# Optimization experiments

Hardware: AMD Instinct MI355X
Metric: run time of the kernel (lower is better)

## Reference

```python
import jax, jax.numpy as jnp
import numpy as np

B, T, D = 4, 2048, 1024
H = 16
HD = D // H  # 64


def setup_inputs() -> dict:
    key = jax.random.key(0)
    ks = jax.random.split(key, 6)
    s = 0.02
    x = jax.random.normal(ks[0], (B, T, D), dtype=jnp.float32)
    # per-head projection weights, stored stacked: [H, HD, D] (torch Linear weight layout)
    Wq = jax.random.normal(ks[1], (H, HD, D), dtype=jnp.float32) * s
    Wk = jax.random.normal(ks[2], (H, HD, D), dtype=jnp.float32) * s
    Wv = jax.random.normal(ks[3], (H, HD, D), dtype=jnp.float32) * s
    Wo = jax.random.normal(ks[4], (D, D), dtype=jnp.float32) * s  # proj weight [out, in]
    bo = jax.random.normal(ks[5], (D,), dtype=jnp.float32) * s
    return {"x": x, "Wq": Wq, "Wk": Wk, "Wv": Wv, "Wo": Wo, "bo": bo}


def reference(x, Wq, Wk, Wv, Wo, bo):
    Bx, Tx, _ = x.shape
    # project: [B,T,D] x [H,HD,D] -> [B,H,T,HD]
    q = jnp.einsum('btd,hed->bhte', x, Wq)
    k = jnp.einsum('btd,hed->bhte', x, Wk)
    v = jnp.einsum('btd,hed->bhte', x, Wv)
    scale = 1.0 / jnp.sqrt(jnp.array(q.shape[-1], dtype=x.dtype))
    scores = jnp.einsum('bhte,bhse->bhts', q, k) * scale  # [B,H,T,T]
    causal = jnp.tril(jnp.ones((Tx, Tx), dtype=bool))
    scores = jnp.where(causal, scores, jnp.array(-jnp.inf, dtype=scores.dtype))
    weights = jax.nn.softmax(scores, axis=-1)
    out = jnp.einsum('bhts,bhse->bhte', weights, v)  # [B,H,T,HD]
    # concat heads (head h occupies contiguous slice, matching torch.cat order)
    out = out.transpose(0, 2, 1, 3).reshape(Bx, Tx, -1)  # [B,T,D]
    out = out @ Wo.T + bo
    return out
```

## Files before the change

### kernel.cpp

```cpp
#include <hip/hip_runtime.h>
#include <cstdint>
#include <cstddef>

typedef unsigned short u16;
typedef float  f32x4  __attribute__((ext_vector_type(4)));
typedef __bf16 bf16x8 __attribute__((ext_vector_type(8)));
typedef unsigned short us8 __attribute__((ext_vector_type(8)));
typedef unsigned short us4 __attribute__((ext_vector_type(4)));
typedef float  f32x4v __attribute__((ext_vector_type(4)));
typedef unsigned int u32x2 __attribute__((ext_vector_type(2)));

#define AS1 __attribute__((address_space(1)))
#define AS3 __attribute__((address_space(3)))

__device__ __forceinline__ u16 f2b(float f) {
  unsigned u = __float_as_uint(f);
  u += 0x7FFFu + ((u >> 16) & 1u);
  return (u16)(u >> 16);
}

__device__ __forceinline__ unsigned pkbf(float a, float b) {
  unsigned ua = __float_as_uint(a) + 0x8000u;
  unsigned ub = __float_as_uint(b) + 0x8000u;
  return __builtin_amdgcn_perm(ub, ua, 0x07060302u);
}

__device__ __forceinline__ bf16x8 ldfrag(const u16* p) {
  us8 v = *(const us8*)p;
  return __builtin_bit_cast(bf16x8, v);
}

__device__ __forceinline__ f32x4 mfma16(bf16x8 a, bf16x8 b, f32x4 c) {
  return __builtin_amdgcn_mfma_f32_16x16x32_bf16(a, b, c, 0, 0, 0);
}

__device__ __forceinline__ void gl_lds16(const u16* g, AS3 u16* l) {
  __builtin_amdgcn_global_load_lds((AS1 void*)g, (AS3 void*)l, 16, 0, 0);
}


__global__ __launch_bounds__(256) void cvt_all(
    const float* __restrict__ x,
    const float* __restrict__ Wq, const float* __restrict__ Wk,
    const float* __restrict__ Wv, const float* __restrict__ Wo,
    u16* __restrict__ xb, u16* __restrict__ Wqkv, u16* __restrict__ Wob) {
  int blk = blockIdx.x;
  const float* s;
  u16* d;
  int i;
  if (blk < 8192)       { s = x;  d = xb;             i = blk * 256 + threadIdx.x; }
  else if (blk < 9216)  { s = Wq; d = Wqkv;           i = (blk - 8192) * 256 + threadIdx.x; }
  else if (blk < 10240) { s = Wk; d = Wqkv + 1048576; i = (blk - 9216) * 256 + threadIdx.x; }
  else if (blk < 11264) { s = Wv; d = Wqkv + 2097152; i = (blk - 10240) * 256 + threadIdx.x; }
  else                  { s = Wo; d = Wob;            i = (blk - 11264) * 256 + threadIdx.x; }
  f32x4v f = ((const f32x4v*)s)[i];
  us4 o = { f2b(f[0]), f2b(f[1]), f2b(f[2]), f2b(f[3]) };
  ((us4*)d)[i] = o;
}

__global__ __launch_bounds__(256) void gemm_qkv(
    const u16* __restrict__ A, const u16* __restrict__ W,
    u16* __restrict__ Qb, u16* __restrict__ Kb, u16* __restrict__ Vt) {
  __shared__ u16 lA[128 * 32];
  __shared__ u16 lB[128 * 32];
  const int tid = threadIdx.x;
  const int lane = tid & 63, wave = tid >> 6;
  const int quad = lane >> 4, l16 = lane & 15;
  const int wr = wave >> 1, wc = wave & 1;
  const int m0 = blockIdx.y * 128;
  const int n0 = blockIdx.x * 128;
  const int sec = n0 >> 10;
  AS3 u16* lA3 = (AS3 u16*)lA;
  AS3 u16* lB3 = (AS3 u16*)lB;
  f32x4 acc[4][4] = {};
  const int swg = (((tid & 3) ^ ((tid >> 3) & 3)) * 8);
  const int qsw = (quad ^ ((l16 >> 1) & 3)) * 8;
  const int ar0 = m0 + (tid >> 2);
  const int br0 = n0 + (tid >> 2);

  const u16* gA0 = A + (size_t)ar0 * 1024 + swg;
  const u16* gA1 = gA0 + 64 * 1024;
  const u16* gB0 = W + (size_t)br0 * 1024 + swg;
  const u16* gB1 = gB0 + 64 * 1024;

  for (int k0 = 0; k0 < 1024; k0 += 32) {
    __syncthreads();
    gl_lds16(gA0 + k0, lA3 + wave * 512);
    gl_lds16(gA1 + k0, lA3 + 2048 + wave * 512);
    gl_lds16(gB0 + k0, lB3 + wave * 512);
    gl_lds16(gB1 + k0, lB3 + 2048 + wave * 512);
    __syncthreads();
    bf16x8 aF[4], bF[4];
#pragma unroll
    for (int mt = 0; mt < 4; mt++)
      aF[mt] = ldfrag(&lA[(wr * 64 + mt * 16 + l16) * 32 + qsw]);
#pragma unroll
    for (int nt = 0; nt < 4; nt++)
      bF[nt] = ldfrag(&lB[(wc * 64 + nt * 16 + l16) * 32 + qsw]);
    if (sec != 2) {
#pragma unroll
      for (int mt = 0; mt < 4; mt++)
#pragma unroll
        for (int nt = 0; nt < 4; nt++)
          acc[mt][nt] = mfma16(aF[mt], bF[nt], acc[mt][nt]);
    } else {
#pragma unroll
      for (int mt = 0; mt < 4; mt++)
#pragma unroll
        for (int nt = 0; nt < 4; nt++)
          acc[mt][nt] = mfma16(bF[nt], aF[mt], acc[mt][nt]);
    }
  }

  if (sec != 2) {
    const float qs = 0.180336880111120426f;
#pragma unroll
    for (int mt = 0; mt < 4; mt++) {
#pragma unroll
      for (int nt = 0; nt < 4; nt++) {
#pragma unroll
        for (int r = 0; r < 4; r++) {
          float v = acc[mt][nt][r];
          int m = m0 + wr * 64 + mt * 16 + quad * 4 + r;
          int n = n0 + wc * 64 + nt * 16 + l16;
          int ns = n & 1023;
          int h = ns >> 6, e = ns & 63;
          int b = m >> 11, t = m & 2047;
          size_t bh = (size_t)b * 16 + h;
          if (sec == 0) Qb[(bh * 2048 + t) * 64 + e] = f2b(v * qs);
          else          Kb[(bh * 2048 + t) * 64 + e] = f2b(v);
        }
      }
    }
  } else {
#pragma unroll
    for (int mt = 0; mt < 4; mt++) {
#pragma unroll
      for (int nt = 0; nt < 4; nt++) {
#pragma unroll
        for (int r = 0; r < 4; r++) {
          float v = acc[mt][nt][r];
          int n = n0 + wc * 64 + nt * 16 + quad * 4 + r;
          int m = m0 + wr * 64 + mt * 16 + l16;
          int ns = n & 1023;
          int h = ns >> 6, e = ns & 63;
          int b = m >> 11, t = m & 2047;
          size_t bh = (size_t)b * 16 + h;
          Vt[(bh * 64 + e) * 2048 + t] = f2b(v);
        }
      }
    }
  }
}

__global__ __launch_bounds__(512, 4) void attn(
    const u16* __restrict__ Q, const u16* __restrict__ K,
    const u16* __restrict__ Vt, u16* __restrict__ O) {
  __shared__ u16 lK[128 * 72];
  __shared__ u16 lV[64 * 136];
  __shared__ u16 lP[8 * 16 * 40];
  const int tid = threadIdx.x;
  const int lane = tid & 63, wave = tid >> 6;
  const int quad = lane >> 4, l16 = lane & 15;
  const int bh = blockIdx.x;
  const int pidx = blockIdx.y;
  const size_t base = (size_t)bh * (2048 * 64);
  u16* lPw = lP + wave * 640;
  const int b = bh >> 4, h = bh & 15;

  for (int half = 0; half < 2; half++) {
    const int qb = half ? pidx : (15 - pidx);
    const int t0 = qb << 7;
    const int tq = t0 + wave * 16 + l16;
    const bf16x8 qF0 = ldfrag(Q + base + (size_t)tq * 64 + quad * 8);
    const bf16x8 qF1 = ldfrag(Q + base + (size_t)tq * 64 + 32 + quad * 8);
    float m_i = -INFINITY, l_i = 0.f;
    f32x4 o[4] = {};

    for (int j = 0; j <= qb; j++) {
      const int s0 = j << 7;
      __syncthreads();
#pragma unroll
      for (int i = 0; i < 2; i++) {
        int c = tid + i * 512;
        int r = c >> 3, col = (c & 7) * 8;
        *(us8*)&lK[r * 72 + col] = *(const us8*)(K + base + (size_t)(s0 + r) * 64 + col);
      }
#pragma unroll
      for (int i = 0; i < 2; i++) {
        int c = tid + i * 512;
        int e = c >> 4, col = (c & 15) * 8;
        *(us8*)&lV[e * 136 + col] = *(const us8*)(Vt + base + (size_t)e * 2048 + s0 + col);
      }
      __syncthreads();

      f32x4 S[8];
      __builtin_amdgcn_s_setprio(1);
#pragma unroll
      for (int nt = 0; nt < 8; nt++) {
        int sr = nt * 16 + l16;
        f32x4 a = {};
        a = mfma16(ldfrag(&lK[sr * 72 + quad * 8]), qF0, a);
        a = mfma16(ldfrag(&lK[sr * 72 + 32 + quad * 8]), qF1, a);
        S[nt] = a;
      }
      __builtin_amdgcn_s_setprio(0);

      if (j == qb) {
#pragma unroll
        for (int nt = 0; nt < 8; nt++)
#pragma unroll
          for (int r = 0; r < 4; r++) {
            int s = s0 + nt * 16 + quad * 4 + r;
            if (s > tq) S[nt][r] = -INFINITY;
          }
      }

      f32x4 m4 = S[0];
#pragma unroll
      for (int nt = 1; nt < 8; nt++)
#pragma unroll
        for (int r = 0; r < 4; r++) m4[r] = fmaxf(m4[r], S[nt][r]);
      float mx = fmaxf(fmaxf(m4[0], m4[1]), fmaxf(m4[2], m4[3]));
      mx = fmaxf(mx, __shfl_xor(mx, 16));
      mx = fmaxf(mx, __shfl_xor(mx, 32));
      float mn = fmaxf(m_i, mx);
      float alpha = __builtin_amdgcn_exp2f(m_i - mn);
      float sum = 0.f;
#pragma unroll
      for (int nt = 0; nt < 8; nt++)
#pragma unroll
        for (int r = 0; r < 4; r++) {
          float p = __builtin_amdgcn_exp2f(S[nt][r] - mn);
          S[nt][r] = p;
          sum += p;
        }
      sum += __shfl_xor(sum, 16);
      sum += __shfl_xor(sum, 32);
      l_i = l_i * alpha + sum;
      m_i = mn;
#pragma unroll
      for (int ot = 0; ot < 4; ot++)
#pragma unroll
        for (int r = 0; r < 4; r++) o[ot][r] *= alpha;

#pragma unroll
      for (int c = 0; c < 4; c++) {
        u32x2 d0 = { pkbf(S[2*c][0],   S[2*c][1]),   pkbf(S[2*c][2],   S[2*c][3]) };
        u32x2 d1 = { pkbf(S[2*c+1][0], S[2*c+1][1]), pkbf(S[2*c+1][2], S[2*c+1][3]) };
        *(u32x2*)&lPw[l16 * 40 + quad * 4]      = d0;
        *(u32x2*)&lPw[l16 * 40 + 16 + quad * 4] = d1;
        __asm__ volatile("s_waitcnt lgkmcnt(0)" ::: "memory");
        bf16x8 bP = ldfrag(&lPw[l16 * 40 + quad * 8]);
        __builtin_amdgcn_s_setprio(1);
#pragma unroll
        for (int ot = 0; ot < 4; ot++)
          o[ot] = mfma16(ldfrag(&lV[(ot * 16 + l16) * 136 + c * 32 + quad * 8]), bP, o[ot]);
        __builtin_amdgcn_s_setprio(0);
      }
    }

    const float inv = 1.f / l_i;
#pragma unroll
    for (int ot = 0; ot < 4; ot++) {
      u32x2 pk = { pkbf(o[ot][0] * inv, o[ot][1] * inv),
                   pkbf(o[ot][2] * inv, o[ot][3] * inv) };
      *(u32x2*)&O[((size_t)b * 2048 + tq) * 1024 + h * 64 + ot * 16 + quad * 4] = pk;
    }
  }
}

__global__ __launch_bounds__(256) void gemm_out(
    const u16* __restrict__ A, const u16* __restrict__ W,
    const float* __restrict__ bias, float* __restrict__ out) {
  __shared__ u16 lA[128 * 32];
  __shared__ u16 lB[128 * 32];
  const int tid = threadIdx.x;
  const int lane = tid & 63, wave = tid >> 6;
  const int quad = lane >> 4, l16 = lane & 15;
  const int wr = wave >> 1, wc = wave & 1;
  const int m0 = blockIdx.y * 128;
  const int n0 = blockIdx.x * 128;
  AS3 u16* lA3 = (AS3 u16*)lA;
  AS3 u16* lB3 = (AS3 u16*)lB;
  f32x4 acc[4][4] = {};
  const int swg = (((tid & 3) ^ ((tid >> 3) & 3)) * 8);
  const int qsw = (quad ^ ((l16 >> 1) & 3)) * 8;
  const int ar0 = m0 + (tid >> 2);
  const int br0 = n0 + (tid >> 2);
  const u16* gA0 = A + (size_t)ar0 * 1024 + swg;
  const u16* gA1 = gA0 + 64 * 1024;
  const u16* gB0 = W + (size_t)br0 * 1024 + swg;
  const u16* gB1 = gB0 + 64 * 1024;

  for (int k0 = 0; k0 < 1024; k0 += 32) {
    __syncthreads();
    gl_lds16(gA0 + k0, lA3 + wave * 512);
    gl_lds16(gA1 + k0, lA3 + 2048 + wave * 512);
    gl_lds16(gB0 + k0, lB3 + wave * 512);
    gl_lds16(gB1 + k0, lB3 + 2048 + wave * 512);
    __syncthreads();
    bf16x8 aF[4], bF[4];
#pragma unroll
    for (int mt = 0; mt < 4; mt++)
      aF[mt] = ldfrag(&lA[(wr * 64 + mt * 16 + l16) * 32 + qsw]);
#pragma unroll
    for (int nt = 0; nt < 4; nt++)
      bF[nt] = ldfrag(&lB[(wc * 64 + nt * 16 + l16) * 32 + qsw]);
#pragma unroll
    for (int mt = 0; mt < 4; mt++)
#pragma unroll
      for (int nt = 0; nt < 4; nt++)
        acc[mt][nt] = mfma16(aF[mt], bF[nt], acc[mt][nt]);
  }

#pragma unroll
  for (int mt = 0; mt < 4; mt++) {
#pragma unroll
    for (int nt = 0; nt < 4; nt++) {
#pragma unroll
      for (int r = 0; r < 4; r++) {
        int m = m0 + wr * 64 + mt * 16 + quad * 4 + r;
        int n = n0 + wc * 64 + nt * 16 + l16;
        out[(size_t)m * 1024 + n] = acc[mt][nt][r] + bias[n];
      }
    }
  }
}

extern "C" void kernel_launch(void* const* d_in, const int* in_sizes, int n_in,
                              void* d_out, int out_size, void* d_ws, size_t ws_size,
                              hipStream_t stream) {
  const float* x  = (const float*)d_in[0];
  const float* Wq = (const float*)d_in[1];
  const float* Wk = (const float*)d_in[2];
  const float* Wv = (const float*)d_in[3];
  const float* Wo = (const float*)d_in[4];
  const float* bo = (const float*)d_in[5];
  float* out = (float*)d_out;

  u16* ws   = (u16*)d_ws;
  u16* xb   = ws;
  u16* Wqkv = ws + 8388608;
  u16* Wob  = ws + 11534336;
  u16* Qb   = ws + 12582912;
  u16* Ao   = xb;
  u16* Kb   = (u16*)d_out;
  u16* Vt   = Kb + 8388608;

  cvt_all<<<12288, 256, 0, stream>>>(x, Wq, Wk, Wv, Wo, xb, Wqkv, Wob);
  gemm_qkv<<<dim3(24, 64), 256, 0, stream>>>(xb, Wqkv, Qb, Kb, Vt);
  attn<<<dim3(64, 8), 512, 0, stream>>>(Qb, Kb, Vt, Ao);
  gemm_out<<<dim3(8, 64), 256, 0, stream>>>(Ao, Wob, bo, out);
}
```

Measured before the change: 259.1 us.

## Rewrite QKV GEMM as 256x256 double-buffered pipelined kernel with block swizzle

Replaces the 128x128 single-buffered QKV projection GEMM with a 512-thread, 256x256-tile kernel. It uses a 128KB double-buffered LDS staging with k-step 64 and interleaves global->LDS loads with quarter-tile MFMA phases, using explicit waitcnt, barriers and setprio. A 1D grid with an XCD-aware block swizzle replaces the 2D launch. The aim is to raise reuse per tile and hide global load latency behind MFMA work. The cost is more register and LDS pressure, only 384 blocks, and fragile manual scheduling.

```diff
diff --git a/kernel.cpp b/kernel.cpp
--- a/kernel.cpp
+++ b/kernel.cpp
@@ -38,6 +38,10 @@
   __builtin_amdgcn_global_load_lds((AS1 void*)g, (AS3 void*)l, 16, 0, 0);
 }
 
+#define BAR()  do { __builtin_amdgcn_s_barrier(); __builtin_amdgcn_sched_barrier(0); } while (0)
+#define WLG()  do { __asm__ volatile("s_waitcnt lgkmcnt(0)" ::: "memory"); __builtin_amdgcn_sched_barrier(0); } while (0)
+#define WVM4() do { __asm__ volatile("s_waitcnt vmcnt(4)" ::: "memory"); __builtin_amdgcn_sched_barrier(0); } while (0)
+#define WVM0() do { __asm__ volatile("s_waitcnt vmcnt(0)" ::: "memory"); __builtin_amdgcn_sched_barrier(0); } while (0)
 
 __global__ __launch_bounds__(256) void cvt_all(
     const float* __restrict__ x,
@@ -58,71 +62,148 @@
   ((us4*)d)[i] = o;
 }
 
-__global__ __launch_bounds__(256) void gemm_qkv(
+__global__ __launch_bounds__(512, 2) void gemm_qkv(
     const u16* __restrict__ A, const u16* __restrict__ W,
     u16* __restrict__ Qb, u16* __restrict__ Kb, u16* __restrict__ Vt) {
-  __shared__ u16 lA[128 * 32];
-  __shared__ u16 lB[128 * 32];
+  __shared__ u16 lds[65536];
   const int tid = threadIdx.x;
   const int lane = tid & 63, wave = tid >> 6;
   const int quad = lane >> 4, l16 = lane & 15;
-  const int wr = wave >> 1, wc = wave & 1;
-  const int m0 = blockIdx.y * 128;
-  const int n0 = blockIdx.x * 128;
+  const int wm = wave >> 2, wn = wave & 3;
+
+  int bid = blockIdx.x;
+  int swz = ((bid & 7) * 48) + (bid >> 3);
+  int by = swz / 12;
+  int bx = swz - by * 12;
+  const int m0 = by * 256, n0 = bx * 256;
   const int sec = n0 >> 10;
-  AS3 u16* lA3 = (AS3 u16*)lA;
-  AS3 u16* lB3 = (AS3 u16*)lB;
-  f32x4 acc[4][4] = {};
-  const int swg = (((tid & 3) ^ ((tid >> 3) & 3)) * 8);
-  const int qsw = (quad ^ ((l16 >> 1) & 3)) * 8;
-  const int ar0 = m0 + (tid >> 2);
-  const int br0 = n0 + (tid >> 2);
-
-  const u16* gA0 = A + (size_t)ar0 * 1024 + swg;
-  const u16* gA1 = gA0 + 64 * 1024;
-  const u16* gB0 = W + (size_t)br0 * 1024 + swg;
-  const u16* gB1 = gB0 + 64 * 1024;
-
-  for (int k0 = 0; k0 < 1024; k0 += 32) {
-    __syncthreads();
-    gl_lds16(gA0 + k0, lA3 + wave * 512);
-    gl_lds16(gA1 + k0, lA3 + 2048 + wave * 512);
-    gl_lds16(gB0 + k0, lB3 + wave * 512);
-    gl_lds16(gB1 + k0, lB3 + 2048 + wave * 512);
-    __syncthreads();
-    bf16x8 aF[4], bF[4];
-#pragma unroll
-    for (int mt = 0; mt < 4; mt++)
-      aF[mt] = ldfrag(&lA[(wr * 64 + mt * 16 + l16) * 32 + qsw]);
-#pragma unroll
-    for (int nt = 0; nt < 4; nt++)
-      bF[nt] = ldfrag(&lB[(wc * 64 + nt * 16 + l16) * 32 + qsw]);
-    if (sec != 2) {
-#pragma unroll
-      for (int mt = 0; mt < 4; mt++)
-#pragma unroll
-        for (int nt = 0; nt < 4; nt++)
-          acc[mt][nt] = mfma16(aF[mt], bF[nt], acc[mt][nt]);
-    } else {
-#pragma unroll
-      for (int mt = 0; mt < 4; mt++)
-#pragma unroll
-        for (int nt = 0; nt < 4; nt++)
-          acc[mt][nt] = mfma16(bF[nt], aF[mt], acc[mt][nt]);
-    }
-  }
+
+  AS3 u16* lds3 = (AS3 u16*)lds;
+
+  const int gsw = (((tid & 7) ^ ((tid >> 3) & 7)) * 8);
+  const int srow = tid >> 3;
+  const u16* gA = A + (size_t)(m0 + srow) * 1024 + gsw;
+  const u16* gB = W + (size_t)(n0 + srow) * 1024 + gsw;
+  const int dst = wave * 512;
+
+  const int p0 = ((quad) ^ (l16 & 7)) * 8;
+  const int p1 = ((4 + quad) ^ (l16 & 7)) * 8;
+  const u16* rdA = lds + wm * 8192 + l16 * 64;
+  const u16* rdB = lds + 16384 + (wn >> 1) * 8192 + ((wn & 1) * 64 + l16) * 64;
+
+#define STAGE_A(kt, h) do {                                             \
+    const u16* s_ = gA + (size_t)(h) * (128 * 1024) + (kt) * 64;        \
+    int d_ = (((kt) & 1) * 32768) + (h) * 8192 + dst;                   \
+    gl_lds16(s_, lds3 + d_);                                            \
+    gl_lds16(s_ + 64 * 1024, lds3 + d_ + 4096);                         \
+  } while (0)
+#define STAGE_B(kt, h) do {                                             \
+    const u16* s_ = gB + (size_t)(h) * (128 * 1024) + (kt) * 64;        \
+    int d_ = (((kt) & 1) * 32768) + 16384 + (h) * 8192 + dst;           \
+    gl_lds16(s_, lds3 + d_);                                            \
+    gl_lds16(s_ + 64 * 1024, lds3 + d_ + 4096);                         \
+  } while (0)
+#define RDA(qm, bufo)                                                   \
+  _Pragma("unroll") for (int t_ = 0; t_ < 4; t_++) {                    \
+    aF[t_][0] = ldfrag(rdA + (bufo) + ((qm) * 4 + t_) * 1024 + p0);     \
+    aF[t_][1] = ldfrag(rdA + (bufo) + ((qm) * 4 + t_) * 1024 + p1);     \
+  }
+#define RDB(BV, qn, bufo)                                               \
+  _Pragma("unroll") for (int u_ = 0; u_ < 2; u_++) {                    \
+    BV[u_][0] = ldfrag(rdB + (bufo) + ((qn) * 2 + u_) * 1024 + p0);     \
+    BV[u_][1] = ldfrag(rdB + (bufo) + ((qn) * 2 + u_) * 1024 + p1);     \
+  }
+#define MM(qm, qn, BV) do {                                             \
+    __builtin_amdgcn_s_setprio(1);                                      \
+    if (sec != 2) {                                                     \
+      _Pragma("unroll") for (int t_ = 0; t_ < 4; t_++)                  \
+      _Pragma("unroll") for (int u_ = 0; u_ < 2; u_++) {                \
+        acc[(qm)*4+t_][(qn)*2+u_] =                                     \
+          mfma16(aF[t_][0], BV[u_][0], acc[(qm)*4+t_][(qn)*2+u_]);      \
+        acc[(qm)*4+t_][(qn)*2+u_] =                                     \
+          mfma16(aF[t_][1], BV[u_][1], acc[(qm)*4+t_][(qn)*2+u_]);      \
+      }                                                                 \
+    } else {                                                            \
+      _Pragma("unroll") for (int t_ = 0; t_ < 4; t_++)                  \
+      _Pragma("unroll") for (int u_ = 0; u_ < 2; u_++) {                \
+        acc[(qm)*4+t_][(qn)*2+u_] =                                     \
+          mfma16(BV[u_][0], aF[t_][0], acc[(qm)*4+t_][(qn)*2+u_]);      \
+        acc[(qm)*4+t_][(qn)*2+u_] =                                     \
+          mfma16(BV[u_][1], aF[t_][1], acc[(qm)*4+t_][(qn)*2+u_]);      \
+      }                                                                 \
+    }                                                                   \
+    __builtin_amdgcn_s_setprio(0);                                      \
+  } while (0)
+
+  f32x4 acc[8][4] = {};
+  bf16x8 aF[4][2], bF[2][2], bQ0[2][2];
+
+  STAGE_A(0, 0); STAGE_A(0, 1); STAGE_B(0, 0); STAGE_B(0, 1);
+  STAGE_B(1, 0); STAGE_B(1, 1);
+  WVM4();
+  BAR();
+
+#pragma unroll 1
+  for (int i = 0; i < 8; i++) {
+    const int kb = 2 * i + 1;
+    RDA(0, 0) RDB(bQ0, 0, 0)
+    STAGE_A(kb, 0);
+    BAR(); WLG();
+    MM(0, 0, bQ0);
+    BAR();
+    RDB(bF, 1, 0)
+    STAGE_A(kb, 1);
+    BAR(); WLG();
+    MM(0, 1, bF);
+    BAR();
+    RDA(1, 0)
+    if (i < 7) STAGE_B(kb + 1, 0);
+    BAR(); WLG();
+    MM(1, 1, bF);
+    BAR();
+    if (i < 7) STAGE_B(kb + 1, 1);
+    BAR();
+    MM(1, 0, bQ0);
+    if (i < 7) { WVM4(); } else { WVM0(); }
+    BAR();
+    RDA(0, 32768) RDB(bQ0, 0, 32768)
+    if (i < 7) STAGE_A(kb + 1, 0);
+    BAR(); WLG();
+    MM(0, 0, bQ0);
+    BAR();
+    RDB(bF, 1, 32768)
+    if (i < 7) STAGE_A(kb + 1, 1);
+    BAR(); WLG();
+    MM(0, 1, bF);
+    BAR();
+    RDA(1, 32768)
+    if (i < 7) STAGE_B(kb + 2, 0);
+    BAR(); WLG();
+    MM(1, 1, bF);
+    BAR();
+    if (i < 7) STAGE_B(kb + 2, 1);
+    BAR();
+    MM(1, 0, bQ0);
+    if (i < 7) { WVM4(); }
+    BAR();
+  }
+#undef STAGE_A
+#undef STAGE_B
+#undef RDA
+#undef RDB
+#undef MM
 
   if (sec != 2) {
     const float qs = 0.180336880111120426f;
 #pragma unroll
-    for (int mt = 0; mt < 4; mt++) {
-#pragma unroll
-      for (int nt = 0; nt < 4; nt++) {
+    for (int mi = 0; mi < 8; mi++) {
+#pragma unroll
+      for (int ni = 0; ni < 4; ni++) {
 #pragma unroll
         for (int r = 0; r < 4; r++) {
-          float v = acc[mt][nt][r];
-          int m = m0 + wr * 64 + mt * 16 + quad * 4 + r;
-          int n = n0 + wc * 64 + nt * 16 + l16;
+          float v = acc[mi][ni][r];
+          int m = m0 + wm * 128 + mi * 16 + quad * 4 + r;
+          int n = n0 + wn * 64 + ni * 16 + l16;
           int ns = n & 1023;
           int h = ns >> 6, e = ns & 63;
           int b = m >> 11, t = m & 2047;
@@ -134,14 +215,14 @@
     }
   } else {
 #pragma unroll
-    for (int mt = 0; mt < 4; mt++) {
-#pragma unroll
-      for (int nt = 0; nt < 4; nt++) {
+    for (int mi = 0; mi < 8; mi++) {
+#pragma unroll
+      for (int ni = 0; ni < 4; ni++) {
 #pragma unroll
         for (int r = 0; r < 4; r++) {
-          float v = acc[mt][nt][r];
-          int n = n0 + wc * 64 + nt * 16 + quad * 4 + r;
-          int m = m0 + wr * 64 + mt * 16 + l16;
+          float v = acc[mi][ni][r];
+          int n = n0 + wn * 64 + ni * 16 + quad * 4 + r;
+          int m = m0 + wm * 128 + mi * 16 + l16;
           int ns = n & 1023;
           int h = ns >> 6, e = ns & 63;
           int b = m >> 11, t = m & 2047;
@@ -349,7 +430,7 @@
   u16* Vt   = Kb + 8388608;
 
   cvt_all<<<12288, 256, 0, stream>>>(x, Wq, Wk, Wv, Wo, xb, Wqkv, Wob);
-  gemm_qkv<<<dim3(24, 64), 256, 0, stream>>>(xb, Wqkv, Qb, Kb, Vt);
+  gemm_qkv<<<384, 512, 0, stream>>>(xb, Wqkv, Qb, Kb, Vt);
   attn<<<dim3(64, 8), 512, 0, stream>>>(Qb, Kb, Vt, Ao);
   gemm_out<<<dim3(8, 64), 256, 0, stream>>>(Ao, Wob, bo, out);
 }
```

Result: slower. 316.0 us (+21.9%).

## Prefetch next K/V tile into registers during attention compute

Applied to the files above, without the earlier changes.

Loads the next K and V tile from global memory into registers while the current tile is being computed, then writes them to shared memory at the start of the next iteration. Barriers and waitcnt are issued by hand with scheduling fences so the global-load latency overlaps the MFMA work. This raises register pressure under launch bounds of 512 threads and 4 blocks, which could cause spills or lower occupancy.

```diff
diff --git a/kernel.cpp b/kernel.cpp
--- a/kernel.cpp
+++ b/kernel.cpp
@@ -168,6 +168,20 @@
   u16* lPw = lP + wave * 640;
   const int b = bh >> 4, h = bh & 15;
 
+  const int c1 = tid + 512;
+  const int rK0 = tid >> 3, cK0 = (tid & 7) * 8;
+  const int rK1 = c1 >> 3,  cK1 = (c1 & 7) * 8;
+  const int eV0 = tid >> 4, cV0 = (tid & 15) * 8;
+  const int eV1 = c1 >> 4,  cV1 = (c1 & 15) * 8;
+  const u16* gK0 = K + base + (size_t)rK0 * 64 + cK0;
+  const u16* gK1 = K + base + (size_t)rK1 * 64 + cK1;
+  const u16* gV0 = Vt + base + (size_t)eV0 * 2048 + cV0;
+  const u16* gV1 = Vt + base + (size_t)eV1 * 2048 + cV1;
+  u16* dK0 = &lK[rK0 * 72 + cK0];
+  u16* dK1 = &lK[rK1 * 72 + cK1];
+  u16* dV0 = &lV[eV0 * 136 + cV0];
+  u16* dV1 = &lV[eV1 * 136 + cV1];
+
   for (int half = 0; half < 2; half++) {
     const int qb = half ? pidx : (15 - pidx);
     const int t0 = qb << 7;
@@ -177,22 +191,30 @@
     float m_i = -INFINITY, l_i = 0.f;
     f32x4 o[4] = {};
 
+    us8 sK0 = *(const us8*)gK0;
+    us8 sK1 = *(const us8*)gK1;
+    us8 sV0 = *(const us8*)gV0;
+    us8 sV1 = *(const us8*)gV1;
+
     for (int j = 0; j <= qb; j++) {
       const int s0 = j << 7;
-      __syncthreads();
-#pragma unroll
-      for (int i = 0; i < 2; i++) {
-        int c = tid + i * 512;
-        int r = c >> 3, col = (c & 7) * 8;
-        *(us8*)&lK[r * 72 + col] = *(const us8*)(K + base + (size_t)(s0 + r) * 64 + col);
-      }
-#pragma unroll
-      for (int i = 0; i < 2; i++) {
-        int c = tid + i * 512;
-        int e = c >> 4, col = (c & 15) * 8;
-        *(us8*)&lV[e * 136 + col] = *(const us8*)(Vt + base + (size_t)e * 2048 + s0 + col);
-      }
-      __syncthreads();
+      __builtin_amdgcn_s_barrier();
+      __builtin_amdgcn_sched_barrier(0);
+      __asm__ volatile("s_waitcnt vmcnt(0)" ::: "memory");
+      __builtin_amdgcn_sched_barrier(0);
+      *(us8*)dK0 = sK0;  *(us8*)dK1 = sK1;
+      *(us8*)dV0 = sV0;  *(us8*)dV1 = sV1;
+      __asm__ volatile("s_waitcnt lgkmcnt(0)" ::: "memory");
+      __builtin_amdgcn_sched_barrier(0);
+      __builtin_amdgcn_s_barrier();
+      __builtin_amdgcn_sched_barrier(0);
+      if (j < qb) {
+        const int sn = (j + 1) << 7;
+        sK0 = *(const us8*)(gK0 + (size_t)sn * 64);
+        sK1 = *(const us8*)(gK1 + (size_t)sn * 64);
+        sV0 = *(const us8*)(gV0 + sn);
+        sV1 = *(const us8*)(gV1 + sn);
+      }
 
       f32x4 S[8];
       __builtin_amdgcn_s_setprio(1);
```

Measured after the change: 273.0 us. 5.3% more time.
